# Performance work log

Measured on AMD Instinct MI355X. Metric: run time of the kernel, lower is better.

## Reference

```python
import jax, jax.numpy as jnp
import numpy as np

B, C = 32, 32768
ENC_DIM, VOCAB, TOK_DIM, HIDDEN = 1024, 100000, 256, 512


def setup_inputs() -> dict:
    key = jax.random.key(0)
    k1, k2, k3, k4, k5 = jax.random.split(key, 5)
    enc_vec = jax.random.normal(k1, (B, ENC_DIM), dtype=jnp.float32)
    cand_tok = jax.random.randint(k2, (B, C), 0, VOCAB, dtype=jnp.int64)
    tok_emb = jax.random.normal(k3, (VOCAB, TOK_DIM), dtype=jnp.float32) * 0.02
    # PAD (0) and BOS (1) rows fixed to zeros, as in __init__
    tok_emb = tok_emb.at[0].set(0.0).at[1].set(0.0)
    W1 = jax.random.normal(k4, (HIDDEN, ENC_DIM), dtype=jnp.float32) * 0.02
    b1 = jnp.zeros((HIDDEN,), dtype=jnp.float32)
    W2 = jax.random.normal(k5, (TOK_DIM, HIDDEN), dtype=jnp.float32) * 0.02
    return {"enc_vec": enc_vec, "cand_tok": cand_tok, "tok_emb": tok_emb,
            "W1": W1, "b1": b1, "W2": W2}


def reference(enc_vec, cand_tok, tok_emb, W1, b1, W2):
    # q_proj: Linear -> GELU (exact, torch default) -> (Dropout inactive at eval) -> Linear (no bias)
    h = jax.nn.gelu(enc_vec @ W1.T + b1, approximate=False)  # (B, hidden)
    q = h @ W2.T                                             # (B, tok_dim)
    Wc = tok_emb[cand_tok]                                   # (B, C, tok_dim) gather
    logits = jnp.einsum('be,bce->bc', q, Wc)                 # (B, C)
    return logits
```

## Files before the change

### kernel.cpp

```cpp
#include <hip/hip_runtime.h>
#include <math.h>

#define B_    32
#define C_    32768
#define ENC_  1024
#define VOCAB_ 100000
#define TOK_  256
#define HID_  512

typedef __attribute__((ext_vector_type(8))) short short8;
typedef __attribute__((ext_vector_type(4))) float f32x4;

__device__ __forceinline__ float gelu_exact(float x) {
    return 0.5f * x * (1.0f + erff(x * 0.70710678118654752f));
}

__device__ __forceinline__ unsigned short f2bf(float f) {
    unsigned u = __builtin_bit_cast(unsigned, f);
    return (unsigned short)((u + 0x7fffu + ((u >> 16) & 1u)) >> 16);
}

__device__ __forceinline__ short8 pack8(float4 a, float4 b) {
    short8 r;
    r[0] = (short)f2bf(a.x); r[1] = (short)f2bf(a.y);
    r[2] = (short)f2bf(a.z); r[3] = (short)f2bf(a.w);
    r[4] = (short)f2bf(b.x); r[5] = (short)f2bf(b.y);
    r[6] = (short)f2bf(b.z); r[7] = (short)f2bf(b.w);
    return r;
}

__global__ __launch_bounds__(256) void k1_hidden(
    const float* __restrict__ enc, const float* __restrict__ W1,
    const float* __restrict__ b1, float* __restrict__ h)
{
    __shared__ float enc_lds[ENC_];
    const int b = blockIdx.y;
    const int tid = threadIdx.x;
    ((float4*)enc_lds)[tid] = ((const float4*)(enc + b * ENC_))[tid];
    __syncthreads();

    const int hw = tid >> 5, lane = tid & 31;
    const int jbase = blockIdx.x * 64 + hw * 8;
    const float4* enc4 = (const float4*)enc_lds;
    #pragma unroll
    for (int i = 0; i < 8; ++i) {
        const int j = jbase + i;
        const float4* wrow = (const float4*)(W1 + (size_t)j * ENC_);
        float acc = 0.f;
        #pragma unroll
        for (int t = 0; t < 8; ++t) {
            const int k4 = t * 32 + lane;
            float4 w = wrow[k4];
            float4 e = enc4[k4];
            acc += w.x * e.x + w.y * e.y + w.z * e.z + w.w * e.w;
        }
        #pragma unroll
        for (int m = 16; m >= 1; m >>= 1) acc += __shfl_xor(acc, m, 32);
        if (lane == 0) h[b * HID_ + j] = gelu_exact(acc + b1[j]);
    }
}

__global__ __launch_bounds__(256) void k2_q(
    const float* __restrict__ h, const float* __restrict__ W2,
    float* __restrict__ q)
{
    __shared__ float h_lds[HID_];
    const int b = blockIdx.y;
    const int tid = threadIdx.x;
    ((float2*)h_lds)[tid] = ((const float2*)(h + b * HID_))[tid];
    __syncthreads();

    const int hw = tid >> 5, lane = tid & 31;
    const int jbase = blockIdx.x * 64 + hw * 8;
    const float4* h4 = (const float4*)h_lds;
    #pragma unroll
    for (int i = 0; i < 8; ++i) {
        const int j = jbase + i;
        const float4* wrow = (const float4*)(W2 + (size_t)j * HID_);
        float acc = 0.f;
        #pragma unroll
        for (int t = 0; t < 4; ++t) {
            const int k4 = t * 32 + lane;
            float4 w = wrow[k4];
            float4 e = h4[k4];
            acc += w.x * e.x + w.y * e.y + w.z * e.z + w.w * e.w;
        }
        #pragma unroll
        for (int m = 16; m >= 1; m >>= 1) acc += __shfl_xor(acc, m, 32);
        if (lane == 0) q[b * TOK_ + j] = acc;
    }
}

__global__ __launch_bounds__(256, 2) void k3_qall_mfma(
    const float* __restrict__ q, const float* __restrict__ tok_emb,
    float* __restrict__ q_allT)
{
    const int wave = (blockIdx.x << 2) + (threadIdx.x >> 6);
    if (wave >= VOCAB_ / 32) return;
    const int lane = threadIdx.x & 63;
    const int m  = lane & 15;
    const int kq = lane >> 4;
    const int v0 = wave * 32;

    short8 bfrag[8][2];
    #pragma unroll
    for (int n = 0; n < 2; ++n) {
        const float* qrow = q + (n * 16 + m) * TOK_ + kq * 8;
        #pragma unroll
        for (int ks = 0; ks < 8; ++ks) {
            const float4* p = (const float4*)(qrow + ks * 32);
            bfrag[ks][n] = pack8(p[0], p[1]);
        }
    }

    f32x4 acc[2][2] = {{{0.f,0.f,0.f,0.f},{0.f,0.f,0.f,0.f}},
                       {{0.f,0.f,0.f,0.f},{0.f,0.f,0.f,0.f}}};
    const float* abase = tok_emb + (size_t)(v0 + m) * TOK_ + kq * 8;
    #pragma unroll
    for (int ks = 0; ks < 8; ++ks) {
        #pragma unroll
        for (int t = 0; t < 2; ++t) {
            const float4* p = (const float4*)(abase + t * 16 * TOK_ + ks * 32);
            short8 afrag = pack8(p[0], p[1]);
            acc[t][0] = __builtin_amdgcn_mfma_f32_16x16x32_bf16(afrag, bfrag[ks][0], acc[t][0], 0, 0, 0);
            acc[t][1] = __builtin_amdgcn_mfma_f32_16x16x32_bf16(afrag, bfrag[ks][1], acc[t][1], 0, 0, 0);
        }
    }

    #pragma unroll
    for (int t = 0; t < 2; ++t) {
        #pragma unroll
        for (int i = 0; i < 4; ++i) {
            const int row = v0 + t * 16 + kq * 4 + i;
            float* dst = q_allT + (size_t)row * B_ + m;
            dst[0]  = acc[t][0][i];
            dst[16] = acc[t][1][i];
        }
    }
}

__global__ __launch_bounds__(256) void k4_gather(
    const int4* __restrict__ cand, const float* __restrict__ q_allT,
    float4* __restrict__ out)
{
    const int i = blockIdx.x * 256 + threadIdx.x;
    const int b = i >> 13;
    const int4 t = cand[i];
    float4 r;
    r.x = q_allT[(size_t)t.x * B_ + b];
    r.y = q_allT[(size_t)t.y * B_ + b];
    r.z = q_allT[(size_t)t.z * B_ + b];
    r.w = q_allT[(size_t)t.w * B_ + b];
    out[i] = r;
}

extern "C" void kernel_launch(void* const* d_in, const int* in_sizes, int n_in,
                              void* d_out, int out_size, void* d_ws, size_t ws_size,
                              hipStream_t stream) {
    const float* enc     = (const float*)d_in[0];
    const int*   cand    = (const int*)  d_in[1];
    const float* tok_emb = (const float*)d_in[2];
    const float* W1      = (const float*)d_in[3];
    const float* b1      = (const float*)d_in[4];
    const float* W2      = (const float*)d_in[5];
    float* out = (float*)d_out;

    float* h      = (float*)d_ws;
    float* q      = h + B_ * HID_;
    float* q_allT = q + B_ * TOK_;

    k1_hidden<<<dim3(8, 32), 256, 0, stream>>>(enc, W1, b1, h);
    k2_q     <<<dim3(4, 32), 256, 0, stream>>>(h, W2, q);

    const int tiles = VOCAB_ / 32;
    k3_qall_mfma<<<(tiles + 3) / 4, 256, 0, stream>>>(q, tok_emb, q_allT);

    k4_gather<<<B_ * C_ / 1024, 256, 0, stream>>>((const int4*)cand, q_allT, (float4*)out);
}
```

Measured before the change: 205.5 us.

## Stage q fragments in LDS, prefetch tok_emb tiles, widen gather per thread

The vocab projection kernel now packs the bf16 q fragments once per block into shared memory, instead of every wave building them in registers. It also double-buffers the next k-slice of tok_emb loads in registers so global loads overlap the MFMAs, and drops the two-blocks-per-CU launch bound. The gather kernel has each thread handle two int4 index vectors (eight outputs), which halves the grid and raises memory-level parallelism per thread. The costs are a block-level sync plus LDS use in the projection, and possibly higher register pressure that could lower occupancy.

```diff
diff --git a/kernel.cpp b/kernel.cpp
--- a/kernel.cpp
+++ b/kernel.cpp
@@ -91,39 +91,60 @@
     }
 }
 
-__global__ __launch_bounds__(256, 2) void k3_qall_mfma(
+__global__ __launch_bounds__(256) void k3_qall_mfma(
     const float* __restrict__ q, const float* __restrict__ tok_emb,
     float* __restrict__ q_allT)
 {
-    const int wave = (blockIdx.x << 2) + (threadIdx.x >> 6);
-    if (wave >= VOCAB_ / 32) return;
-    const int lane = threadIdx.x & 63;
+    __shared__ short8 q_lds[1024];
+    const int tid  = threadIdx.x;
+    const int lane = tid & 63;
+    const int hw   = tid >> 6;
     const int m  = lane & 15;
     const int kq = lane >> 4;
+
+    #pragma unroll
+    for (int ks2 = 0; ks2 < 2; ++ks2) {
+        const int ks = hw * 2 + ks2;
+        #pragma unroll
+        for (int n = 0; n < 2; ++n) {
+            const float4* p = (const float4*)(q + (n * 16 + m) * TOK_ + ks * 32 + kq * 8);
+            q_lds[(ks * 2 + n) * 64 + lane] = pack8(p[0], p[1]);
+        }
+    }
+    __syncthreads();
+
+    const int wave = blockIdx.x * 4 + hw;
+    if (wave >= VOCAB_ / 32) return;
     const int v0 = wave * 32;
 
-    short8 bfrag[8][2];
-    #pragma unroll
-    for (int n = 0; n < 2; ++n) {
-        const float* qrow = q + (n * 16 + m) * TOK_ + kq * 8;
-        #pragma unroll
-        for (int ks = 0; ks < 8; ++ks) {
-            const float4* p = (const float4*)(qrow + ks * 32);
-            bfrag[ks][n] = pack8(p[0], p[1]);
-        }
+    const float* abase = tok_emb + (size_t)(v0 + m) * TOK_ + kq * 8;
+
+    float4 st[2][4];
+    #pragma unroll
+    for (int t = 0; t < 2; ++t) {
+        st[0][t * 2 + 0] = *(const float4*)(abase + t * 16 * TOK_);
+        st[0][t * 2 + 1] = *(const float4*)(abase + t * 16 * TOK_ + 4);
     }
 
     f32x4 acc[2][2] = {{{0.f,0.f,0.f,0.f},{0.f,0.f,0.f,0.f}},
                        {{0.f,0.f,0.f,0.f},{0.f,0.f,0.f,0.f}}};
-    const float* abase = tok_emb + (size_t)(v0 + m) * TOK_ + kq * 8;
     #pragma unroll
     for (int ks = 0; ks < 8; ++ks) {
+        const int cur = ks & 1, nxt = cur ^ 1;
+        if (ks < 7) {
+            #pragma unroll
+            for (int t = 0; t < 2; ++t) {
+                st[nxt][t * 2 + 0] = *(const float4*)(abase + t * 16 * TOK_ + (ks + 1) * 32);
+                st[nxt][t * 2 + 1] = *(const float4*)(abase + t * 16 * TOK_ + (ks + 1) * 32 + 4);
+            }
+        }
+        short8 b0 = q_lds[(ks * 2 + 0) * 64 + lane];
+        short8 b1 = q_lds[(ks * 2 + 1) * 64 + lane];
         #pragma unroll
         for (int t = 0; t < 2; ++t) {
-            const float4* p = (const float4*)(abase + t * 16 * TOK_ + ks * 32);
-            short8 afrag = pack8(p[0], p[1]);
-            acc[t][0] = __builtin_amdgcn_mfma_f32_16x16x32_bf16(afrag, bfrag[ks][0], acc[t][0], 0, 0, 0);
-            acc[t][1] = __builtin_amdgcn_mfma_f32_16x16x32_bf16(afrag, bfrag[ks][1], acc[t][1], 0, 0, 0);
+            short8 af = pack8(st[cur][t * 2 + 0], st[cur][t * 2 + 1]);
+            acc[t][0] = __builtin_amdgcn_mfma_f32_16x16x32_bf16(af, b0, acc[t][0], 0, 0, 0);
+            acc[t][1] = __builtin_amdgcn_mfma_f32_16x16x32_bf16(af, b1, acc[t][1], 0, 0, 0);
         }
     }
 
@@ -144,14 +165,20 @@
     float4* __restrict__ out)
 {
     const int i = blockIdx.x * 256 + threadIdx.x;
-    const int b = i >> 13;
-    const int4 t = cand[i];
-    float4 r;
-    r.x = q_allT[(size_t)t.x * B_ + b];
-    r.y = q_allT[(size_t)t.y * B_ + b];
-    r.z = q_allT[(size_t)t.z * B_ + b];
-    r.w = q_allT[(size_t)t.w * B_ + b];
-    out[i] = r;
+    const int b = i >> 12;
+    const int4 c0 = cand[i * 2];
+    const int4 c1 = cand[i * 2 + 1];
+    float4 r0, r1;
+    r0.x = q_allT[(size_t)c0.x * B_ + b];
+    r0.y = q_allT[(size_t)c0.y * B_ + b];
+    r0.z = q_allT[(size_t)c0.z * B_ + b];
+    r0.w = q_allT[(size_t)c0.w * B_ + b];
+    r1.x = q_allT[(size_t)c1.x * B_ + b];
+    r1.y = q_allT[(size_t)c1.y * B_ + b];
+    r1.z = q_allT[(size_t)c1.z * B_ + b];
+    r1.w = q_allT[(size_t)c1.w * B_ + b];
+    out[i * 2]     = r0;
+    out[i * 2 + 1] = r1;
 }
 
 extern "C" void kernel_launch(void* const* d_in, const int* in_sizes, int n_in,
@@ -175,5 +202,5 @@
     const int tiles = VOCAB_ / 32;
     k3_qall_mfma<<<(tiles + 3) / 4, 256, 0, stream>>>(q, tok_emb, q_allT);
 
-    k4_gather<<<B_ * C_ / 1024, 256, 0, stream>>>((const int4*)cand, q_allT, (float4*)out);
-}
+    k4_gather<<<B_ * C_ / 2048, 256, 0, stream>>>((const int4*)cand, q_allT, (float4*)out);
+}
```

New measurement: 205.0 us. Within noise of the previous version (-0.2%).
